# Kernel optimization log

Hardware: AMD Instinct MI355X
Metric: run time of the kernel (lower is better)

## Reference

```python
import jax, jax.numpy as jnp
import numpy as np

N = 50000
E = 800000
H = 96
NUM_IN = 11
PE_DIM = 24
NUM_OUT = 1
NUM_LAYERS = 4
NUM_GRAPHS = 256


def _linear_params(key, d_in, d_out):
    k1, k2 = jax.random.split(key)
    bound = 1.0 / np.sqrt(d_in)
    w = jax.random.uniform(k1, (d_in, d_out), jnp.float32, -bound, bound)
    b = jax.random.uniform(k2, (d_out,), jnp.float32, -bound, bound)
    return w, b


def setup_inputs() -> dict:
    key = jax.random.key(0)
    ks = jax.random.split(key, 32)
    x = jax.random.normal(ks[0], (N, NUM_IN), jnp.float32)
    pos = jax.random.normal(ks[1], (N, 3), jnp.float32)
    pe = jax.random.normal(ks[2], (N, PE_DIM), jnp.float32)
    edge_index = jax.random.randint(ks[3], (2, E), 0, N, jnp.int64)
    batch = jnp.sort(jax.random.randint(ks[4], (N,), 0, NUM_GRAPHS, jnp.int64))
    embed_w1, embed_b1 = _linear_params(ks[5], NUM_IN + PE_DIM, H)
    embed_w2, embed_b2 = _linear_params(ks[6], H, H)
    # per-layer stacked params
    msg_w1 = []; msg_b1 = []; msg_w2 = []; msg_b2 = []
    upd_w1 = []; upd_b1 = []; upd_w2 = []; upd_b2 = []
    for l in range(NUM_LAYERS):
        w, b = _linear_params(ks[7 + l], 2 * H + 1, H); msg_w1.append(w); msg_b1.append(b)
        w, b = _linear_params(ks[11 + l], H, H); msg_w2.append(w); msg_b2.append(b)
        w, b = _linear_params(ks[15 + l], 2 * H, H); upd_w1.append(w); upd_b1.append(b)
        w, b = _linear_params(ks[19 + l], H, H); upd_w2.append(w); upd_b2.append(b)
    pre_w1, pre_b1 = _linear_params(ks[23], H, H)
    pre_w2, pre_b2 = _linear_params(ks[24], H, H)
    ro_w1, ro_b1 = _linear_params(ks[25], H, H)
    ro_w2, ro_b2 = _linear_params(ks[26], H, NUM_OUT)
    return {
        'x': x, 'pos': pos, 'pe': pe, 'edge_index': edge_index, 'batch': batch,
        'embed_w1': embed_w1, 'embed_b1': embed_b1, 'embed_w2': embed_w2, 'embed_b2': embed_b2,
        'msg_w1': jnp.stack(msg_w1), 'msg_b1': jnp.stack(msg_b1),
        'msg_w2': jnp.stack(msg_w2), 'msg_b2': jnp.stack(msg_b2),
        'upd_w1': jnp.stack(upd_w1), 'upd_b1': jnp.stack(upd_b1),
        'upd_w2': jnp.stack(upd_w2), 'upd_b2': jnp.stack(upd_b2),
        'pre_w1': pre_w1, 'pre_b1': pre_b1, 'pre_w2': pre_w2, 'pre_b2': pre_b2,
        'ro_w1': ro_w1, 'ro_b1': ro_b1, 'ro_w2': ro_w2, 'ro_b2': ro_b2,
    }


def _egnn_forward(x, pos, pe, edge_index, batch,
                  embed_w1, embed_b1, embed_w2, embed_b2,
                  msg_w1, msg_b1, msg_w2, msg_b2,
                  upd_w1, upd_b1, upd_w2, upd_b2,
                  pre_w1, pre_b1, pre_w2, pre_b2,
                  ro_w1, ro_b1, ro_w2, ro_b2):
    silu = jax.nn.silu
    send, rec = edge_index[0], edge_index[1]
    h = jnp.concatenate([x, pe], axis=-1)
    h = silu(h @ embed_w1 + embed_b1) @ embed_w2 + embed_b2  # [N,H]
    dist = jnp.linalg.norm(pos[send] - pos[rec], axis=1)[:, None]  # [E,1]
    for l in range(NUM_LAYERS):
        state = jnp.concatenate([h[send], h[rec], dist], axis=1)  # [E,2H+1]
        msg = silu(silu(state @ msg_w1[l] + msg_b1[l]) @ msg_w2[l] + msg_b2[l])  # [E,H]
        aggr = jax.ops.segment_sum(msg, rec, num_segments=h.shape[0])  # [N,H]
        upd_in = jnp.concatenate([h, aggr], axis=1)
        update = silu(upd_in @ upd_w1[l] + upd_b1[l]) @ upd_w2[l] + upd_b2[l]
        h = h + update
    h = silu(h @ pre_w1 + pre_b1) @ pre_w2 + pre_b2
    pooled = jax.ops.segment_sum(h, batch, num_segments=NUM_GRAPHS)  # [G,H]
    out = silu(pooled @ ro_w1 + ro_b1) @ ro_w2 + ro_b2  # [G,1]
    return jnp.squeeze(out)


def reference(x, pos, pe, edge_index, batch,
              embed_w1, embed_b1, embed_w2, embed_b2,
              msg_w1, msg_b1, msg_w2, msg_b2,
              upd_w1, upd_b1, upd_w2, upd_b2,
              pre_w1, pre_b1, pre_w2, pre_b2,
              ro_w1, ro_b1, ro_w2, ro_b2):
    return _egnn_forward(x, pos, pe, edge_index, batch,
                         embed_w1, embed_b1, embed_w2, embed_b2,
                         msg_w1, msg_b1, msg_w2, msg_b2,
                         upd_w1, upd_b1, upd_w2, upd_b2,
                         pre_w1, pre_b1, pre_w2, pre_b2,
                         ro_w1, ro_b1, ro_w2, ro_b2)
```

## Files before the change

kernel.cpp:

```cpp
#include <hip/hip_runtime.h>
#include <hip/hip_bf16.h>

#define HDIM 96
#define TILE 128
#define NTILE 64

typedef __attribute__((ext_vector_type(8))) short  short8;
typedef __attribute__((ext_vector_type(4))) short  short4v;
typedef __attribute__((ext_vector_type(4))) float  float4v;
typedef __attribute__((ext_vector_type(2))) float  float2v;
typedef __attribute__((ext_vector_type(4))) unsigned int uint4v;
typedef __attribute__((ext_vector_type(2))) unsigned int uint2v;

static __device__ __forceinline__ short f2bf(float f){
    unsigned u = __float_as_uint(f);
    return (short)((u + 0x8000u) >> 16);
}
static __device__ __forceinline__ float bf2f(short s){
    unsigned u = ((unsigned)(unsigned short)s) << 16;
    return __uint_as_float(u);
}
static __device__ __forceinline__ float silu_f(float v){
    return v * __builtin_amdgcn_rcpf(1.0f + __expf(-v));
}
static __device__ __forceinline__ unsigned silu2_pack(float2v v){
    float e0 = __expf(-v[0]);
    float e1 = __expf(-v[1]);
    float2v ep = {e0, e1};
    const float2v one2 = {1.0f, 1.0f};
    ep += one2;
    float2v q = { __builtin_amdgcn_rcpf(ep[0]), __builtin_amdgcn_rcpf(ep[1]) };
    float2v res = v * q;
    unsigned pa = __float_as_uint(res[0]) + 0x8000u;
    unsigned pb = __float_as_uint(res[1]) + 0x8000u;
    return __builtin_amdgcn_perm(pb, pa, 0x07060302);
}

typedef __attribute__((address_space(1))) const unsigned int guint;
typedef __attribute__((address_space(3))) unsigned int luint;
static __device__ __forceinline__ void gload_lds16(const void* g, void* l){
    __builtin_amdgcn_global_load_lds((guint*)g, (luint*)l, 16, 0, 0);
}

struct SwJob { const float* src; int ck; int ks; int ksrc; };
struct SwTable { SwJob j[22]; };

__global__ __launch_bounds__(256) void swizzle_all(SwTable T, const float* __restrict__ msg_w1,
                                                   short* __restrict__ dst, short* __restrict__ dst2,
                                                   int total1, int total2){
    int gid = blockIdx.x*256 + threadIdx.x;
    if (gid < total1) {
        int ksg = gid / 3072;
        int e   = gid % 3072;
        const float* src = T.j[0].src; int k0 = 0, ksrc = 0;
        #pragma unroll
        for (int jj = 0; jj < 22; ++jj){
            int s = T.j[jj].ck;
            if (ksg >= s && ksg < s + T.j[jj].ks){ src = T.j[jj].src; k0 = (ksg - s)*32; ksrc = T.j[jj].ksrc; }
        }
        int nt   = e >> 9;
        int rem  = e & 511;
        int lane = rem >> 3;
        int jx   = rem & 7;
        int k = k0 + ((lane >> 4) << 3) + jx;
        int f = nt*16 + (lane & 15);
        float v = (k < ksrc) ? src[(size_t)k*HDIM + f] : 0.0f;
        dst[gid] = f2bf(v);
    } else if (gid < total1 + total2) {
        int g2 = gid - total1;
        int layer = g2 / 18432;
        int e     = g2 % 18432;
        int ksg = e / 6144;
        int rem = e % 6144;
        int nt   = rem >> 9;
        int r2   = rem & 511;
        int lane = r2 >> 3;
        int jx   = r2 & 7;
        int k = ksg*32 + ((lane >> 4) << 3) + jx;
        int f = nt*16 + (lane & 15);
        int row = (f < 96) ? k : (96 + k);
        int col = (f < 96) ? f : (f - 96);
        dst2[g2] = f2bf(msg_w1[(size_t)layer*193*96 + (size_t)row*96 + col]);
    }
}

__global__ __launch_bounds__(256) void hist_kernel(const int* __restrict__ rec, int* __restrict__ deg, int E){
    int e = blockIdx.x*256 + threadIdx.x;
    if (e < E) atomicAdd(&deg[rec[e]], 1);
}

__global__ __launch_bounds__(256) void scan_part(const int* __restrict__ deg, int* __restrict__ part, int N){
    __shared__ int red[256];
    const int t = threadIdx.x;
    int base = blockIdx.x*1024;
    int s = 0;
    #pragma unroll
    for (int j=0;j<4;j++){ int i = base + j*256 + t; s += (i<N)?deg[i]:0; }
    red[t]=s; __syncthreads();
    #pragma unroll
    for (int off=128; off>0; off>>=1){ if (t<off) red[t]+=red[t+off]; __syncthreads(); }
    if (t==0) part[blockIdx.x]=red[0];
}
__global__ __launch_bounds__(256) void scan_top(int* __restrict__ part, int nb){
    __shared__ int buf[256];
    const int t = threadIdx.x;
    int v = (t < nb) ? part[t] : 0;
    buf[t] = v;
    __syncthreads();
    #pragma unroll
    for (int off=1; off<256; off<<=1){
        int u = (t>=off)?buf[t-off]:0;
        __syncthreads();
        buf[t] += u;
        __syncthreads();
    }
    if (t < nb) part[t] = buf[t] - v;
}
__global__ __launch_bounds__(256) void scan_final(const int* __restrict__ deg, const int* __restrict__ part,
                                                  int* __restrict__ cur, int N){
    __shared__ int tsum[256];
    const int t = threadIdx.x;
    int i0 = blockIdx.x*1024 + t*4;
    int a0 = (i0+0<N)?deg[i0+0]:0;
    int a1 = (i0+1<N)?deg[i0+1]:0;
    int a2 = (i0+2<N)?deg[i0+2]:0;
    int a3 = (i0+3<N)?deg[i0+3]:0;
    int s = a0+a1+a2+a3;
    tsum[t]=s; __syncthreads();
    #pragma unroll
    for (int off=1; off<256; off<<=1){
        int u = (t>=off)?tsum[t-off]:0;
        __syncthreads();
        tsum[t]+=u;
        __syncthreads();
    }
    int excl = tsum[t]-s + part[blockIdx.x];
    if (i0+0<N) cur[i0+0]=excl;
    if (i0+1<N) cur[i0+1]=excl+a0;
    if (i0+2<N) cur[i0+2]=excl+a0+a1;
    if (i0+3<N) cur[i0+3]=excl+a0+a1+a2;
}

__global__ __launch_bounds__(256) void scatter_kernel(
    const int* __restrict__ send, const int* __restrict__ rec, const float* __restrict__ pos,
    int* __restrict__ cur, int2* __restrict__ sd_s, int* __restrict__ rec_s, int E)
{
    int e = blockIdx.x*256 + threadIdx.x;
    if (e >= E) return;
    int s = send[e], r = rec[e];
    int p = atomicAdd(&cur[r], 1);
    float dx = pos[3*s]   - pos[3*r];
    float dy = pos[3*s+1] - pos[3*r+1];
    float dz = pos[3*s+2] - pos[3*r+2];
    float d = sqrtf(dx*dx + dy*dy + dz*dz);
    sd_s[p] = make_int2(s, __float_as_int(d));
    rec_s[p] = r;
}

__global__ __launch_bounds__(256,5) void edge_kernel(
    const short* __restrict__ SR,
    const int2* __restrict__ sd_s, const int* __restrict__ rec_s,
    const float* __restrict__ w1r192,
    const short* __restrict__ w2sw, const float* __restrict__ b2,
    float* __restrict__ aggr, float* __restrict__ stageA, float* __restrict__ stageB, int E)
{
    __shared__ short msgS[TILE*104];
    __shared__ int   recS[TILE];
    __shared__ int   startIdxS[TILE+1];
    __shared__ int   wcntS[2];
    const int t  = threadIdx.x;
    const int e0 = blockIdx.x * TILE;
    const int lane = t & 63;
    const int wv   = t >> 6;
    const int e_lo = wv * 32;
    const int col  = lane & 15;
    const int quad = lane >> 4;
    const int frow = quad * 4;
    const float4v fzero = {0.f,0.f,0.f,0.f};

    int seStage[7], ccStage[7];
    #pragma unroll
    for (int i=0;i<7;i++){
        int idx = i*4 + wv;
        if (idx < 26){
            int s  = idx*64 + lane;
            int es = s/13;
            int cc = s - es*13; if (cc > 11) cc = 11;
            int ec = e0 + es; if (ec >= E) ec = E - 1;
            seStage[i] = ((const int*)sd_s)[2*ec];
            ccStage[i] = cc;
        }
    }
    #pragma unroll
    for (int i=0;i<7;i++){
        int idx = i*4 + wv;
        if (idx < 26){
            const short* src = SR + (size_t)seStage[i]*192 + ccStage[i]*8;
            gload_lds16(src, msgS + idx*512);
        }
    }

    int re[2]; float dd[2];
    #pragma unroll
    for (int et=0; et<2; ++et){
        int ec = e0 + e_lo + et*16 + col; if (ec >= E) ec = E - 1;
        int2 sd = sd_s[ec];
        dd[et] = __int_as_float(sd.y);
        re[et] = rec_s[ec];
    }
    uint4v Rvu[2][3];
    #pragma unroll
    for (int et=0; et<2; ++et)
      #pragma unroll
      for (int ks=0; ks<3; ++ks){
        int f0 = ks*32 + quad*8;
        Rvu[et][ks] = *(const uint4v*)(SR + (size_t)re[et]*192 + 96 + f0);
      }

    int myRec = 0;
    bool flag = false;
    if (t < TILE) {
        int e = e0 + t; if (e >= E) e = E - 1;
        myRec = rec_s[e];
        recS[t] = myRec;
        int ep = e0 + t - 1; if (ep >= E) ep = E - 1;
        flag = (t == 0) || (myRec != rec_s[ep]);
    }
    unsigned long long bmask = __ballot(flag ? 1 : 0);
    int pre = __popcll(bmask & ((1ull << (t & 63)) - 1ull));
    if (t < TILE && (t & 63) == 0) wcntS[t >> 6] = __popcll(bmask);

    const bool firstB = (e0 > 0) && (rec_s[e0-1] == rec_s[e0]);
    const bool lastB  = (e0 + TILE < E) && (rec_s[e0 + TILE] == rec_s[(e0+TILE-1 < E)? e0+TILE-1 : E-1]);

    __syncthreads();

    if (flag) startIdxS[pre + ((t >> 6) ? wcntS[0] : 0)] = t;
    if (t == 0) startIdxS[wcntS[0] + wcntS[1]] = TILE;

    short8 frag[2][3];
    #pragma unroll
    for (int et=0; et<2; ++et){
        float2v d2 = {dd[et], dd[et]};
        int e_local = e_lo + et*16 + col;
        #pragma unroll
        for (int ks=0; ks<3; ++ks){
            int f0 = ks*32 + quad*8;
            float4v wa = *(const float4v*)(w1r192 + f0);
            float4v wb = *(const float4v*)(w1r192 + f0 + 4);
            uint4v su = *(const uint4v*)(msgS + e_local*104 + (ks*4+quad)*8);
            uint4v ru = Rvu[et][ks];
            uint4v fo;
            #pragma unroll
            for (int p=0;p<4;p++){
                float2v w2;
                if      (p==0) w2 = (float2v){wa[0], wa[1]};
                else if (p==1) w2 = (float2v){wa[2], wa[3]};
                else if (p==2) w2 = (float2v){wb[0], wb[1]};
                else           w2 = (float2v){wb[2], wb[3]};
                unsigned us = su[p], ur = ru[p];
                float2v s2 = { __uint_as_float(us << 16), __uint_as_float(us & 0xffff0000u) };
                float2v r2 = { __uint_as_float(ur << 16), __uint_as_float(ur & 0xffff0000u) };
                float2v v = s2 + r2 + d2*w2;
                fo[p] = silu2_pack(v);
            }
            short8 fr;
            __builtin_memcpy(&fr, &fo, 16);
            frag[et][ks] = fr;
        }
    }
    __syncthreads();

    float4v acc2[2][6];
    #pragma unroll
    for (int i=0;i<2;i++)
      #pragma unroll
      for (int n=0;n<6;n++) acc2[i][n] = fzero;

    const short8* w2f = (const short8*)w2sw;
    #pragma unroll
    for (int ks = 0; ks < 3; ++ks) {
        #pragma unroll
        for (int mt = 0; mt < 6; ++mt) {
            short8 a = w2f[(ks*6+mt)*64 + lane];
            acc2[0][mt] = __builtin_amdgcn_mfma_f32_16x16x32_bf16(a, frag[0][ks], acc2[0][mt], 0, 0, 0);
            acc2[1][mt] = __builtin_amdgcn_mfma_f32_16x16x32_bf16(a, frag[1][ks], acc2[1][mt], 0, 0, 0);
        }
    }
    float4v b2v[6];
    #pragma unroll
    for (int mt=0; mt<6; ++mt) b2v[mt] = *(const float4v*)(b2 + mt*16 + frow);

    #pragma unroll
    for (int et=0; et<2; ++et){
        int e = e_lo + et*16 + col;
        bool valid = (e0 + e) < E;
        #pragma unroll
        for (int mt=0; mt<6; ++mt){
            float2v vlo = { acc2[et][mt][0] + b2v[mt][0], acc2[et][mt][1] + b2v[mt][1] };
            float2v vhi = { acc2[et][mt][2] + b2v[mt][2], acc2[et][mt][3] + b2v[mt][3] };
            unsigned ulo = silu2_pack(vlo);
            unsigned uhi = silu2_pack(vhi);
            if (!valid){ ulo = 0u; uhi = 0u; }
            uint2v st = {ulo, uhi};
            *(uint2v*)(msgS + e*104 + mt*16 + frow) = st;
        }
    }
    __syncthreads();

    const int nseg = wcntS[0] + wcntS[1];
    const int items = nseg * 24;
    for (int item = t; item < items; item += 256){
        int s  = item / 24;
        int fg = item - s*24;
        int r0 = startIdxS[s], r1 = startIdxS[s+1];
        float2v s01 = {0.f,0.f}, s23 = {0.f,0.f};
        for (int r = r0; r < r1; ++r){
            const unsigned* pp = (const unsigned*)(msgS + r*104 + fg*4);
            unsigned p0 = pp[0], p1 = pp[1];
            float2v a0 = { __uint_as_float(p0 << 16), __uint_as_float(p0 & 0xffff0000u) };
            float2v a1 = { __uint_as_float(p1 << 16), __uint_as_float(p1 & 0xffff0000u) };
            s01 += a0; s23 += a1;
        }
        int node = recS[r0];
        float* dstp;
        if (s == 0 && firstB)            dstp = stageB + (size_t)node*HDIM + fg*4;
        else if (s == nseg-1 && lastB)   dstp = stageA + (size_t)node*HDIM + fg*4;
        else                             dstp = aggr   + (size_t)node*HDIM + fg*4;
        float4v v = {s01[0], s01[1], s23[0], s23[1]};
        *(float4v*)(dstp) = v;
    }
}

__global__ __launch_bounds__(256,3) void update_kernel(
    short* __restrict__ hbf, const float* __restrict__ aggr,
    const float* __restrict__ stageA, const float* __restrict__ stageB,
    const int* __restrict__ deg, const int* __restrict__ cur,
    const short* __restrict__ w1sw, const float* __restrict__ b1,
    const short* __restrict__ w2sw, const float* __restrict__ b2,
    const short* __restrict__ w1sr_next, const float* __restrict__ msgb1_next,
    short* __restrict__ SR,
    const short* __restrict__ pw1, const float* __restrict__ pb1,
    const short* __restrict__ pw2, const float* __restrict__ pb2,
    const int* __restrict__ batch, float* __restrict__ pooled, int N)
{
    __shared__ short stateS[NTILE*208];
    __shared__ int   batchS[NTILE];
    __shared__ int   startIdxS[NTILE+1];
    __shared__ int   nsegS;
    const int t  = threadIdx.x;
    const int n0 = blockIdx.x * NTILE;

    #pragma unroll
    for (int it = 0; it < 6; ++it) {
        int q = it*256 + t;
        int c = q % 24;
        int i = q / 24;
        int node = n0 + i;
        if (c < 12) {
            uint4v v = {0u,0u,0u,0u};
            if (node < N) v = *(const uint4v*)(hbf + (size_t)node*HDIM + c*8);
            *(uint4v*)(stateS + i*200 + c*8) = v;
        } else {
            int cc = c - 12;
            short8 s8 = {0,0,0,0,0,0,0,0};
            if (node < N) {
                int dg = deg[node];
                int en = cur[node];
                int st = en - dg;
                bool bnd = (dg > 0) && (st/TILE != (en-1)/TILE);
                float4v a0, a1;
                if (bnd) {
                    size_t b = (size_t)node*HDIM + cc*8;
                    a0 = *(const float4v*)(stageA + b)     + *(const float4v*)(stageB + b);
                    a1 = *(const float4v*)(stageA + b + 4) + *(const float4v*)(stageB + b + 4);
                } else {
                    a0 = *(const float4v*)(aggr + (size_t)node*HDIM + cc*8);
                    a1 = *(const float4v*)(aggr + (size_t)node*HDIM + cc*8 + 4);
                }
                s8[0]=f2bf(a0[0]); s8[1]=f2bf(a0[1]); s8[2]=f2bf(a0[2]); s8[3]=f2bf(a0[3]);
                s8[4]=f2bf(a1[0]); s8[5]=f2bf(a1[1]); s8[6]=f2bf(a1[2]); s8[7]=f2bf(a1[3]);
            }
            *(short8*)(stateS + i*200 + HDIM + cc*8) = s8;
        }
    }
    __syncthreads();

    const int lane = t & 63;
    const int wv   = t >> 6;
    const int rb   = wv * 16;
    const int col  = lane & 15;
    const int quad = lane >> 4;
    const int koff = quad * 8;
    const int frow = quad * 4;
    const float4v fzero = {0.f,0.f,0.f,0.f};

    float4v acc[6];
    #pragma unroll
    for (int n=0;n<6;n++) acc[n] = fzero;

    const short8* w1f = (const short8*)w1sw;
    #pragma unroll
    for (int ks = 0; ks < 6; ++ks) {
        short8 bb = *(const short8*)(stateS + (rb+col)*200 + ks*32 + koff);
        #pragma unroll
        for (int mt = 0; mt < 6; ++mt) {
            short8 a = w1f[(ks*6+mt)*64 + lane];
            acc[mt] = __builtin_amdgcn_mfma_f32_16x16x32_bf16(a, bb, acc[mt], 0, 0, 0);
        }
    }
    float4v b1v[6];
    #pragma unroll
    for (int mt=0; mt<6; ++mt) b1v[mt] = *(const float4v*)(b1 + mt*16 + frow);
    __syncthreads();

    short* t1S = stateS;
    {
        int e = rb + col;
        #pragma unroll
        for (int mt=0; mt<6; ++mt){
            short4v sv;
            #pragma unroll
            for (int r=0;r<4;r++) sv[r] = f2bf(silu_f(acc[mt][r] + b1v[mt][r]));
            *(short4v*)(t1S + e*104 + mt*16 + frow) = sv;
        }
    }
    __syncthreads();

    float4v acc2[6];
    #pragma unroll
    for (int n=0;n<6;n++) acc2[n] = fzero;

    const short8* w2f = (const short8*)w2sw;
    #pragma unroll
    for (int ks = 0; ks < 3; ++ks) {
        short8 bb = *(const short8*)(t1S + (rb+col)*104 + ks*32 + koff);
        #pragma unroll
        for (int mt = 0; mt < 6; ++mt) {
            short8 a = w2f[(ks*6+mt)*64 + lane];
            acc2[mt] = __builtin_amdgcn_mfma_f32_16x16x32_bf16(a, bb, acc2[mt], 0, 0, 0);
        }
    }
    float4v b2v[6];
    #pragma unroll
    for (int mt=0; mt<6; ++mt) b2v[mt] = *(const float4v*)(b2 + mt*16 + frow);
    __syncthreads();

    {
        int erow = rb + col;
        int node = n0 + erow;
        bool valid = node < N;
        size_t base = (size_t)node*HDIM;
        #pragma unroll
        for (int mt=0; mt<6; ++mt){
            int f0 = mt*16 + frow;
            short4v ov = {0,0,0,0};
            if (valid) ov = *(const short4v*)(hbf + base + f0);
            float4v o;
            #pragma unroll
            for (int r=0;r<4;r++) o[r] = bf2f(ov[r]) + acc2[mt][r] + b2v[mt][r];
            short4v sv = {f2bf(o[0]), f2bf(o[1]), f2bf(o[2]), f2bf(o[3])};
            if (valid) *(short4v*)(hbf + base + f0) = sv;
            *(short4v*)(stateS + erow*104 + f0) = sv;
        }
    }

    if (w1sr_next) {
        __syncthreads();
        float4v accS[12];
        #pragma unroll
        for (int n=0;n<12;n++) accS[n] = fzero;

        const short8* wsf = (const short8*)w1sr_next;
        #pragma unroll
        for (int ks = 0; ks < 3; ++ks) {
            short8 bb = *(const short8*)(stateS + (rb+col)*104 + ks*32 + koff);
            #pragma unroll
            for (int mt = 0; mt < 12; ++mt) {
                short8 a = wsf[(ks*12+mt)*64 + lane];
                accS[mt] = __builtin_amdgcn_mfma_f32_16x16x32_bf16(a, bb, accS[mt], 0, 0, 0);
            }
        }
        float4v bnv[6];
        #pragma unroll
        for (int mt=0; mt<6; ++mt) bnv[mt] = *(const float4v*)(msgb1_next + mt*16 + frow);

        {
            int node = n0 + rb + col;
            if (node < N) {
                size_t sbase = (size_t)node*192;
                #pragma unroll
                for (int mt=0; mt<12; ++mt){
                    float4v o = accS[mt];
                    if (mt < 6) { o[0]+=bnv[mt][0]; o[1]+=bnv[mt][1]; o[2]+=bnv[mt][2]; o[3]+=bnv[mt][3]; }
                    short4v sv = {f2bf(o[0]), f2bf(o[1]), f2bf(o[2]), f2bf(o[3])};
                    *(short4v*)(SR + sbase + mt*16 + frow) = sv;
                }
            }
        }
    } else if (pw1) {
        if (t < NTILE) {
            int node = n0 + t;
            batchS[t] = batch[node < N ? node : N-1];
        }
        __syncthreads();

        bool flag = false;
        if (t < NTILE) flag = (t == 0) || (batchS[t] != batchS[t-1]);
        unsigned long long bm = __ballot(flag ? 1 : 0);
        if (t < NTILE) {
            int pre = __popcll(bm & ((1ull << t) - 1ull));
            if (flag) startIdxS[pre] = t;
            if (t == 0) nsegS = __popcll(bm);
        }

        float4v accp[6];
        #pragma unroll
        for (int n=0;n<6;n++) accp[n] = fzero;

        const short8* pw1f = (const short8*)pw1;
        #pragma unroll
        for (int ks = 0; ks < 3; ++ks) {
            short8 bb = *(const short8*)(stateS + (rb+col)*104 + ks*32 + koff);
            #pragma unroll
            for (int mt = 0; mt < 6; ++mt) {
                short8 a = pw1f[(ks*6+mt)*64 + lane];
                accp[mt] = __builtin_amdgcn_mfma_f32_16x16x32_bf16(a, bb, accp[mt], 0, 0, 0);
            }
        }
        float4v pb1v[6];
        #pragma unroll
        for (int mt=0; mt<6; ++mt) pb1v[mt] = *(const float4v*)(pb1 + mt*16 + frow);

        short* t1p = stateS + NTILE*104;
        {
            int e = rb + col;
            #pragma unroll
            for (int mt=0; mt<6; ++mt){
                short4v sv;
                #pragma unroll
                for (int r=0;r<4;r++) sv[r] = f2bf(silu_f(accp[mt][r] + pb1v[mt][r]));
                *(short4v*)(t1p + e*104 + mt*16 + frow) = sv;
            }
        }
        __syncthreads();

        float4v accq[6];
        #pragma unroll
        for (int n=0;n<6;n++) accq[n] = fzero;

        const short8* pw2f = (const short8*)pw2;
        #pragma unroll
        for (int ks = 0; ks < 3; ++ks) {
            short8 bb = *(const short8*)(t1p + (rb+col)*104 + ks*32 + koff);
            #pragma unroll
            for (int mt = 0; mt < 6; ++mt) {
                short8 a = pw2f[(ks*6+mt)*64 + lane];
                accq[mt] = __builtin_amdgcn_mfma_f32_16x16x32_bf16(a, bb, accq[mt], 0, 0, 0);
            }
        }
        float4v pb2v[6];
        #pragma unroll
        for (int mt=0; mt<6; ++mt) pb2v[mt] = *(const float4v*)(pb2 + mt*16 + frow);
        __syncthreads();

        float* msgS = (float*)stateS;
        {
            int e = rb + col;
            bool valid = (n0 + e) < N;
            #pragma unroll
            for (int mt=0; mt<6; ++mt){
                float4v v;
                #pragma unroll
                for (int r=0;r<4;r++){
                    float u = accq[mt][r] + pb2v[mt][r];
                    v[r] = valid ? u : 0.0f;
                }
                *(float4v*)(msgS + e*100 + mt*16 + frow) = v;
            }
        }
        __syncthreads();

        const int nseg = nsegS;
        if (t == 0) startIdxS[nseg] = NTILE;
        __syncthreads();

        const int items = nseg * 24;
        for (int item = t; item < items; item += 256){
            int s  = item / 24;
            int fg = item - s*24;
            int r0 = startIdxS[s], r1 = startIdxS[s+1];
            float4v sum = fzero;
            for (int r = r0; r < r1; ++r) sum += *(const float4v*)(msgS + r*100 + fg*4);
            float* dstp = pooled + (size_t)batchS[r0]*HDIM + fg*4;
            atomicAdd(dstp+0, sum[0]);
            atomicAdd(dstp+1, sum[1]);
            atomicAdd(dstp+2, sum[2]);
            atomicAdd(dstp+3, sum[3]);
        }
    }
}

__global__ __launch_bounds__(256,3) void embed_kernel(
    const float* __restrict__ x, const float* __restrict__ pe,
    const short* __restrict__ w1sw, const float* __restrict__ b1,
    const short* __restrict__ w2sw, const float* __restrict__ b2,
    short* __restrict__ hbf,
    const short* __restrict__ w1sr0, const float* __restrict__ msgb1_0,
    short* __restrict__ SR, int N)
{
    __shared__ short stateS[NTILE*72];
    __shared__ short t1S[NTILE*104];
    const int t  = threadIdx.x;
    const int n0 = blockIdx.x * NTILE;

    if (t < NTILE) {
        int node = n0 + t;
        short* row = stateS + t*72;
        if (node < N) {
            #pragma unroll
            for (int j=0;j<11;j++) row[j]    = f2bf(x[(size_t)node*11 + j]);
            #pragma unroll
            for (int j=0;j<24;j++) row[11+j] = f2bf(pe[(size_t)node*24 + j]);
            #pragma unroll
            for (int j=35;j<64;j++) row[j] = 0;
        } else {
            #pragma unroll
            for (int j=0;j<64;j++) row[j] = 0;
        }
    }
    __syncthreads();

    const int lane = t & 63;
    const int wv   = t >> 6;
    const int rb   = wv * 16;
    const int col  = lane & 15;
    const int quad = lane >> 4;
    const int koff = quad * 8;
    const int frow = quad * 4;
    const float4v fzero = {0.f,0.f,0.f,0.f};

    float4v acc[6];
    #pragma unroll
    for (int n=0;n<6;n++) acc[n] = fzero;

    const short8* w1f = (const short8*)w1sw;
    #pragma unroll
    for (int ks = 0; ks < 2; ++ks) {
        short8 bb = *(const short8*)(stateS + (rb+col)*72 + ks*32 + koff);
        #pragma unroll
        for (int mt = 0; mt < 6; ++mt) {
            short8 a = w1f[(ks*6+mt)*64 + lane];
            acc[mt] = __builtin_amdgcn_mfma_f32_16x16x32_bf16(a, bb, acc[mt], 0, 0, 0);
        }
    }
    float4v b1v[6];
    #pragma unroll
    for (int mt=0; mt<6; ++mt) b1v[mt] = *(const float4v*)(b1 + mt*16 + frow);

    {
        int e = rb + col;
        #pragma unroll
        for (int mt=0; mt<6; ++mt){
            short4v sv;
            #pragma unroll
            for (int r=0;r<4;r++) sv[r] = f2bf(silu_f(acc[mt][r] + b1v[mt][r]));
            *(short4v*)(t1S + e*104 + mt*16 + frow) = sv;
        }
    }
    __syncthreads();

    float4v acc2[6];
    #pragma unroll
    for (int n=0;n<6;n++) acc2[n] = fzero;

    const short8* w2f = (const short8*)w2sw;
    #pragma unroll
    for (int ks = 0; ks < 3; ++ks) {
        short8 bb = *(const short8*)(t1S + (rb+col)*104 + ks*32 + koff);
        #pragma unroll
        for (int mt = 0; mt < 6; ++mt) {
            short8 a = w2f[(ks*6+mt)*64 + lane];
            acc2[mt] = __builtin_amdgcn_mfma_f32_16x16x32_bf16(a, bb, acc2[mt], 0, 0, 0);
        }
    }
    float4v b2v[6];
    #pragma unroll
    for (int mt=0; mt<6; ++mt) b2v[mt] = *(const float4v*)(b2 + mt*16 + frow);
    __syncthreads();

    {
        int erow = rb + col;
        int node = n0 + erow;
        bool valid = node < N;
        size_t base = (size_t)node*HDIM;
        #pragma unroll
        for (int mt=0; mt<6; ++mt){
            int f0 = mt*16 + frow;
            float4v o;
            #pragma unroll
            for (int r=0;r<4;r++) o[r] = acc2[mt][r] + b2v[mt][r];
            short4v sv = {f2bf(o[0]), f2bf(o[1]), f2bf(o[2]), f2bf(o[3])};
            if (valid) *(short4v*)(hbf + base + f0) = sv;
            *(short4v*)(t1S + erow*104 + f0) = sv;
        }
    }
    __syncthreads();

    float4v accS[12];
    #pragma unroll
    for (int n=0;n<12;n++) accS[n] = fzero;

    const short8* wsf = (const short8*)w1sr0;
    #pragma unroll
    for (int ks = 0; ks < 3; ++ks) {
        short8 bb = *(const short8*)(t1S + (rb+col)*104 + ks*32 + koff);
        #pragma unroll
        for (int mt = 0; mt < 12; ++mt) {
            short8 a = wsf[(ks*12+mt)*64 + lane];
            accS[mt] = __builtin_amdgcn_mfma_f32_16x16x32_bf16(a, bb, accS[mt], 0, 0, 0);
        }
    }
    float4v bnv[6];
    #pragma unroll
    for (int mt=0; mt<6; ++mt) bnv[mt] = *(const float4v*)(msgb1_0 + mt*16 + frow);

    {
        int node = n0 + rb + col;
        if (node < N) {
            size_t sbase = (size_t)node*192;
            #pragma unroll
            for (int mt=0; mt<12; ++mt){
                float4v o = accS[mt];
                if (mt < 6) { o[0]+=bnv[mt][0]; o[1]+=bnv[mt][1]; o[2]+=bnv[mt][2]; o[3]+=bnv[mt][3]; }
                short4v sv = {f2bf(o[0]), f2bf(o[1]), f2bf(o[2]), f2bf(o[3])};
                *(short4v*)(SR + sbase + mt*16 + frow) = sv;
            }
        }
    }
}

__global__ __launch_bounds__(128) void readout_kernel(
    const float* __restrict__ pooled,
    const float* __restrict__ w1, const float* __restrict__ b1,
    const float* __restrict__ w2, const float* __restrict__ b2,
    float* __restrict__ out)
{
    __shared__ float red[128];
    const int g = blockIdx.x;
    const int t = threadIdx.x;
    float p = 0.0f;
    if (t < HDIM) {
        float acc = b1[t];
        for (int k = 0; k < HDIM; ++k)
            acc += pooled[(size_t)g*HDIM + k] * w1[(size_t)k*HDIM + t];
        acc = silu_f(acc);
        p = acc * w2[t];
    }
    red[t] = p;
    __syncthreads();
    for (int s = 64; s > 0; s >>= 1) {
        if (t < s) red[t] += red[t + s];
        __syncthreads();
    }
    if (t == 0) out[g] = red[0] + b2[0];
}

extern "C" void kernel_launch(void* const* d_in, const int* in_sizes, int n_in,
                              void* d_out, int out_size, void* d_ws, size_t ws_size,
                              hipStream_t stream)
{
    const float* x        = (const float*)d_in[0];
    const float* pos      = (const float*)d_in[1];
    const float* pe       = (const float*)d_in[2];
    const int*   ei       = (const int*)d_in[3];
    const int*   batch    = (const int*)d_in[4];
    const float* embed_w1 = (const float*)d_in[5];
    const float* embed_b1 = (const float*)d_in[6];
    const float* embed_w2 = (const float*)d_in[7];
    const float* embed_b2 = (const float*)d_in[8];
    const float* msg_w1   = (const float*)d_in[9];
    const float* msg_b1   = (const float*)d_in[10];
    const float* msg_w2   = (const float*)d_in[11];
    const float* msg_b2   = (const float*)d_in[12];
    const float* upd_w1   = (const float*)d_in[13];
    const float* upd_b1   = (const float*)d_in[14];
    const float* upd_w2   = (const float*)d_in[15];
    const float* upd_b2   = (const float*)d_in[16];
    const float* pre_w1   = (const float*)d_in[17];
    const float* pre_b1   = (const float*)d_in[18];
    const float* pre_w2   = (const float*)d_in[19];
    const float* pre_b2   = (const float*)d_in[20];
    const float* ro_w1    = (const float*)d_in[21];
    const float* ro_b1    = (const float*)d_in[22];
    const float* ro_w2    = (const float*)d_in[23];
    const float* ro_b2    = (const float*)d_in[24];

    const int E = in_sizes[3] / 2;
    const int N = in_sizes[4];
    const int G = out_size;

    char* ws = (char*)d_ws;
    size_t off = 0;
    auto alloc = [&](size_t bytes){ void* p = ws + off; off += (bytes + 255) & ~(size_t)255; return p; };
    short* hbf    = (short*)alloc((size_t)N*HDIM*2);
    float* aggr   = (float*)alloc((size_t)N*HDIM*4);
    float* stageA = (float*)alloc((size_t)N*HDIM*4);
    float* stageB = (float*)alloc((size_t)N*HDIM*4);
    float* pooled = (float*)alloc((size_t)G*HDIM*4);
    short* wsw    = (short*)alloc((size_t)59*3072*2);
    short* w1sr   = (short*)alloc((size_t)4*18432*2);
    short* SR     = (short*)alloc((size_t)N*192*2);
    int*   deg    = (int*)alloc((size_t)N*4);
    int*   cur    = (int*)alloc((size_t)N*4);
    int*   part   = (int*)alloc((size_t)256*4);
    int2*  sd_s   = (int2*)alloc((size_t)E*8);
    int*   rec_s  = (int*)alloc((size_t)E*4);

    hipMemsetAsync(aggr,   0, (size_t)N*HDIM*4, stream);
    hipMemsetAsync(pooled, 0, (size_t)G*HDIM*4, stream);
    hipMemsetAsync(deg,    0, (size_t)N*4, stream);

    SwTable T;
    for (int jj=0;jj<22;jj++){ T.j[jj].src = embed_w1; T.j[jj].ck = 1<<30; T.j[jj].ks = 0; T.j[jj].ksrc = 0; }
    int ck = 0, ji = 0;
    auto add = [&](const float* s, int ks, int ksrc){
        T.j[ji].src = s; T.j[ji].ck = ck; T.j[ji].ks = ks; T.j[ji].ksrc = ksrc;
        ji++; ck += ks;
    };
    add(embed_w1, 2, 35);
    add(embed_w2, 3, 96);
    add(pre_w1,   3, 96);
    add(pre_w2,   3, 96);
    for (int l=0;l<4;l++) add(msg_w2 + (size_t)l*96*96,  3, 96);
    for (int l=0;l<4;l++) add(upd_w1 + (size_t)l*192*96, 6, 192);
    for (int l=0;l<4;l++) add(upd_w2 + (size_t)l*96*96,  3, 96);
    const int total1 = 59*3072;
    const int total2 = 4*18432;
    swizzle_all<<<(total1+total2+255)/256, 256, 0, stream>>>(T, msg_w1, wsw, w1sr, total1, total2);

    const int nbE256 = (E + 255) / 256;
    const int nbScan = (N + 1023) / 1024;
    hist_kernel<<<nbE256, 256, 0, stream>>>(ei + E, deg, E);
    scan_part<<<nbScan, 256, 0, stream>>>(deg, part, N);
    scan_top<<<1, 256, 0, stream>>>(part, nbScan);
    scan_final<<<nbScan, 256, 0, stream>>>(deg, part, cur, N);
    scatter_kernel<<<nbE256, 256, 0, stream>>>(ei, ei + E, pos, cur, sd_s, rec_s, E);

    const int nbN = (N + NTILE - 1) / NTILE;
    embed_kernel<<<nbN, 256, 0, stream>>>(x, pe, wsw + 0, embed_b1, wsw + 2*3072, embed_b2,
                                          hbf, w1sr, msg_b1, SR, N);

    const int nbE = (E + TILE - 1) / TILE;
    for (int l = 0; l < 4; ++l) {
        edge_kernel<<<nbE, 256, 0, stream>>>(SR, sd_s, rec_s,
            msg_w1 + (size_t)l*193*96 + (size_t)192*96,
            wsw + (11 + 3*l)*3072, msg_b2 + l*96, aggr, stageA, stageB, E);
        const short* w1sr_next  = (l < 3) ? (w1sr + (size_t)(l+1)*18432) : nullptr;
        const float* msgb1_next = (l < 3) ? (msg_b1 + (l+1)*96) : nullptr;
        const short* pw1 = (l == 3) ? (wsw + 5*3072) : nullptr;
        const float* pb1 = (l == 3) ? pre_b1 : nullptr;
        const short* pw2 = (l == 3) ? (wsw + 8*3072) : nullptr;
        const float* pb2 = (l == 3) ? pre_b2 : nullptr;
        update_kernel<<<nbN, 256, 0, stream>>>(hbf, aggr, stageA, stageB, deg, cur,
            wsw + (23 + 6*l)*3072, upd_b1 + l*96,
            wsw + (47 + 3*l)*3072, upd_b2 + l*96,
            w1sr_next, msgb1_next, SR,
            pw1, pb1, pw2, pb2, batch, pooled, N);
    }

    readout_kernel<<<G, 128, 0, stream>>>(pooled, ro_w1, ro_b1, ro_w2, ro_b2, (float*)d_out);
}
```

Before: 716.7 us.

## Fold memsets into swizzle kernel, relayout edge LDS staging, specialize full tiles

Removes the three hipMemsetAsync calls and has the swizzle kernel zero aggr, pooled and deg with float4 stores. The edge kernel's sender-feature staging moves from a per-edge row layout (stride 104, 26 chunks) to a chunk-major layout (24 chunks of 128x8), which simplifies the gather index math and the LDS reads. The edge body is templated on whether the tile is full, so interior tiles skip the bounds clamps. Weight loads and bias adds use float2 vector forms. The deg zeroing writes float4 over (N+3)/4 entries, which relies on the allocation being padded.

```diff
diff --git a/kernel.cpp b/kernel.cpp
--- a/kernel.cpp
+++ b/kernel.cpp
@@ -47,7 +47,9 @@
 
 __global__ __launch_bounds__(256) void swizzle_all(SwTable T, const float* __restrict__ msg_w1,
                                                    short* __restrict__ dst, short* __restrict__ dst2,
-                                                   int total1, int total2){
+                                                   int total1, int total2,
+                                                   float* __restrict__ aggrZ, float* __restrict__ pooledZ,
+                                                   int* __restrict__ degZ, int nA, int nP, int nD){
     int gid = blockIdx.x*256 + threadIdx.x;
     if (gid < total1) {
         int ksg = gid / 3072;
@@ -81,6 +83,12 @@
         int row = (f < 96) ? k : (96 + k);
         int col = (f < 96) ? f : (f - 96);
         dst2[g2] = f2bf(msg_w1[(size_t)layer*193*96 + (size_t)row*96 + col]);
+    } else {
+        int gz = gid - total1 - total2;
+        const float4v z = {0.f,0.f,0.f,0.f};
+        if (gz < nA)                 ((float4v*)aggrZ)[gz] = z;
+        else if (gz < nA + nP)       ((float4v*)pooledZ)[gz - nA] = z;
+        else if (gz < nA + nP + nD)  ((float4v*)degZ)[gz - nA - nP] = z;
     }
 }
 
@@ -157,17 +165,15 @@
     rec_s[p] = r;
 }
 
-__global__ __launch_bounds__(256,5) void edge_kernel(
+template<bool FULL>
+static __device__ __forceinline__ void edge_body(
     const short* __restrict__ SR,
     const int2* __restrict__ sd_s, const int* __restrict__ rec_s,
     const float* __restrict__ w1r192,
     const short* __restrict__ w2sw, const float* __restrict__ b2,
-    float* __restrict__ aggr, float* __restrict__ stageA, float* __restrict__ stageB, int E)
+    float* __restrict__ aggr, float* __restrict__ stageA, float* __restrict__ stageB, int E,
+    short* msgS, int* recS, int* startIdxS, int* wcntS)
 {
-    __shared__ short msgS[TILE*104];
-    __shared__ int   recS[TILE];
-    __shared__ int   startIdxS[TILE+1];
-    __shared__ int   wcntS[2];
     const int t  = threadIdx.x;
     const int e0 = blockIdx.x * TILE;
     const int lane = t & 63;
@@ -177,33 +183,31 @@
     const int quad = lane >> 4;
     const int frow = quad * 4;
     const float4v fzero = {0.f,0.f,0.f,0.f};
-
-    int seStage[7], ccStage[7];
-    #pragma unroll
-    for (int i=0;i<7;i++){
+    const int emax = E - 1;
+
+    int seStage[6];
+    const int* sdp = (const int*)sd_s;
+    #pragma unroll
+    for (int i=0;i<6;i++){
         int idx = i*4 + wv;
-        if (idx < 26){
-            int s  = idx*64 + lane;
-            int es = s/13;
-            int cc = s - es*13; if (cc > 11) cc = 11;
-            int ec = e0 + es; if (ec >= E) ec = E - 1;
-            seStage[i] = ((const int*)sd_s)[2*ec];
-            ccStage[i] = cc;
-        }
-    }
-    #pragma unroll
-    for (int i=0;i<7;i++){
+        int e  = ((idx & 1) << 6) + lane;
+        int ec = e0 + e;
+        if (!FULL) ec = min(ec, emax);
+        seStage[i] = sdp[2*ec];
+    }
+    #pragma unroll
+    for (int i=0;i<6;i++){
         int idx = i*4 + wv;
-        if (idx < 26){
-            const short* src = SR + (size_t)seStage[i]*192 + ccStage[i]*8;
-            gload_lds16(src, msgS + idx*512);
-        }
+        int cc  = idx >> 1;
+        const short* src = SR + (size_t)seStage[i]*192 + cc*8;
+        gload_lds16(src, msgS + idx*512);
     }
 
     int re[2]; float dd[2];
     #pragma unroll
     for (int et=0; et<2; ++et){
-        int ec = e0 + e_lo + et*16 + col; if (ec >= E) ec = E - 1;
+        int ec = e0 + e_lo + et*16 + col;
+        if (!FULL) ec = min(ec, emax);
         int2 sd = sd_s[ec];
         dd[et] = __int_as_float(sd.y);
         re[et] = rec_s[ec];
@@ -220,10 +224,12 @@
     int myRec = 0;
     bool flag = false;
     if (t < TILE) {
-        int e = e0 + t; if (e >= E) e = E - 1;
+        int e = e0 + t;
+        if (!FULL) e = min(e, emax);
         myRec = rec_s[e];
         recS[t] = myRec;
-        int ep = e0 + t - 1; if (ep >= E) ep = E - 1;
+        int ep = e0 + t - 1;
+        if (!FULL && ep > emax) ep = emax;
         flag = (t == 0) || (myRec != rec_s[ep]);
     }
     unsigned long long bmask = __ballot(flag ? 1 : 0);
@@ -231,7 +237,7 @@
     if (t < TILE && (t & 63) == 0) wcntS[t >> 6] = __popcll(bmask);
 
     const bool firstB = (e0 > 0) && (rec_s[e0-1] == rec_s[e0]);
-    const bool lastB  = (e0 + TILE < E) && (rec_s[e0 + TILE] == rec_s[(e0+TILE-1 < E)? e0+TILE-1 : E-1]);
+    const bool lastB  = (e0 + TILE < E) && (rec_s[e0 + TILE] == rec_s[FULL ? (e0+TILE-1) : min(e0+TILE-1, emax)]);
 
     __syncthreads();
 
@@ -246,18 +252,13 @@
         #pragma unroll
         for (int ks=0; ks<3; ++ks){
             int f0 = ks*32 + quad*8;
-            float4v wa = *(const float4v*)(w1r192 + f0);
-            float4v wb = *(const float4v*)(w1r192 + f0 + 4);
-            uint4v su = *(const uint4v*)(msgS + e_local*104 + (ks*4+quad)*8);
+            const float2v* wp = (const float2v*)(w1r192 + f0);
+            uint4v su = *(const uint4v*)(msgS + (ks*4+quad)*1024 + e_local*8);
             uint4v ru = Rvu[et][ks];
             uint4v fo;
             #pragma unroll
             for (int p=0;p<4;p++){
-                float2v w2;
-                if      (p==0) w2 = (float2v){wa[0], wa[1]};
-                else if (p==1) w2 = (float2v){wa[2], wa[3]};
-                else if (p==2) w2 = (float2v){wb[0], wb[1]};
-                else           w2 = (float2v){wb[2], wb[3]};
+                float2v w2 = wp[p];
                 unsigned us = su[p], ur = ru[p];
                 float2v s2 = { __uint_as_float(us << 16), __uint_as_float(us & 0xffff0000u) };
                 float2v r2 = { __uint_as_float(ur << 16), __uint_as_float(ur & 0xffff0000u) };
@@ -294,13 +295,15 @@
     #pragma unroll
     for (int et=0; et<2; ++et){
         int e = e_lo + et*16 + col;
-        bool valid = (e0 + e) < E;
+        bool valid = FULL || ((e0 + e) < E);
         #pragma unroll
         for (int mt=0; mt<6; ++mt){
-            float2v vlo = { acc2[et][mt][0] + b2v[mt][0], acc2[et][mt][1] + b2v[mt][1] };
-            float2v vhi = { acc2[et][mt][2] + b2v[mt][2], acc2[et][mt][3] + b2v[mt][3] };
-            unsigned ulo = silu2_pack(vlo);
-            unsigned uhi = silu2_pack(vhi);
+            float2v aLo = *(const float2v*)&acc2[et][mt];
+            float2v aHi = *((const float2v*)&acc2[et][mt] + 1);
+            float2v bLo = *(const float2v*)&b2v[mt];
+            float2v bHi = *((const float2v*)&b2v[mt] + 1);
+            unsigned ulo = silu2_pack(aLo + bLo);
+            unsigned uhi = silu2_pack(aHi + bHi);
             if (!valid){ ulo = 0u; uhi = 0u; }
             uint2v st = {ulo, uhi};
             *(uint2v*)(msgS + e*104 + mt*16 + frow) = st;
@@ -330,6 +333,24 @@
         float4v v = {s01[0], s01[1], s23[0], s23[1]};
         *(float4v*)(dstp) = v;
     }
+}
+
+__global__ __launch_bounds__(256,5) void edge_kernel(
+    const short* __restrict__ SR,
+    const int2* __restrict__ sd_s, const int* __restrict__ rec_s,
+    const float* __restrict__ w1r192,
+    const short* __restrict__ w2sw, const float* __restrict__ b2,
+    float* __restrict__ aggr, float* __restrict__ stageA, float* __restrict__ stageB, int E)
+{
+    __shared__ short msgS[TILE*104];
+    __shared__ int   recS[TILE];
+    __shared__ int   startIdxS[TILE+1];
+    __shared__ int   wcntS[2];
+    const int e0 = blockIdx.x * TILE;
+    if (e0 + TILE <= E)
+        edge_body<true >(SR, sd_s, rec_s, w1r192, w2sw, b2, aggr, stageA, stageB, E, msgS, recS, startIdxS, wcntS);
+    else
+        edge_body<false>(SR, sd_s, rec_s, w1r192, w2sw, b2, aggr, stageA, stageB, E, msgS, recS, startIdxS, wcntS);
 }
 
 __global__ __launch_bounds__(256,3) void update_kernel(
@@ -817,10 +838,6 @@
     int2*  sd_s   = (int2*)alloc((size_t)E*8);
     int*   rec_s  = (int*)alloc((size_t)E*4);
 
-    hipMemsetAsync(aggr,   0, (size_t)N*HDIM*4, stream);
-    hipMemsetAsync(pooled, 0, (size_t)G*HDIM*4, stream);
-    hipMemsetAsync(deg,    0, (size_t)N*4, stream);
-
     SwTable T;
     for (int jj=0;jj<22;jj++){ T.j[jj].src = embed_w1; T.j[jj].ck = 1<<30; T.j[jj].ks = 0; T.j[jj].ksrc = 0; }
     int ck = 0, ji = 0;
@@ -837,7 +854,12 @@
     for (int l=0;l<4;l++) add(upd_w2 + (size_t)l*96*96,  3, 96);
     const int total1 = 59*3072;
     const int total2 = 4*18432;
-    swizzle_all<<<(total1+total2+255)/256, 256, 0, stream>>>(T, msg_w1, wsw, w1sr, total1, total2);
+    const int nA = N*24;
+    const int nP = G*24;
+    const int nD = (N+3)/4;
+    const int totalZ = nA + nP + nD;
+    swizzle_all<<<(total1+total2+totalZ+255)/256, 256, 0, stream>>>(T, msg_w1, wsw, w1sr, total1, total2,
+                                                                   aggr, pooled, deg, nA, nP, nD);
 
     const int nbE256 = (E + 255) / 256;
     const int nbScan = (N + 1023) / 1024;
```

Result: no change. 709.1 us (-1.0%).
